# Optimization experiments

Measured on AMD Instinct MI355X. Metric: run time of the kernel, lower is better.

The kernel has to match this reference:

```python
import math
import jax, jax.numpy as jnp
import numpy as np

S, M, B, D, H = 256, 256, 8, 512, 8
HD = D // H
K = S + M  # key_len


def setup_inputs() -> dict:
    key = jax.random.key(0)
    ks = jax.random.split(key, 10)
    x = jax.random.normal(ks[0], (S, B, D), jnp.float32)
    memory = jax.random.normal(ks[1], (M, B, D), jnp.float32)
    rel_pos = jax.random.normal(ks[2], (K, D), jnp.float32)
    # causal mask: True means masked (key position after query position)
    q_pos = jnp.arange(S)[:, None] + M  # (S,1)
    k_pos = jnp.arange(K)[None, :]     # (1,K)
    attn_mask = jnp.broadcast_to(k_pos > q_pos, (B, S, K))
    scale = 1.0 / math.sqrt(D)
    Wq = jax.random.normal(ks[3], (D, D), jnp.float32) * scale
    Wk = jax.random.normal(ks[4], (D, D), jnp.float32) * scale
    Wv = jax.random.normal(ks[5], (D, D), jnp.float32) * scale
    Wr = jax.random.normal(ks[6], (D, D), jnp.float32) * scale
    Wo = jax.random.normal(ks[7], (D, D), jnp.float32) * scale
    u_bias = jax.random.normal(ks[8], (H, HD), jnp.float32) * 0.02
    v_bias = jax.random.normal(ks[9], (H, HD), jnp.float32) * 0.02
    return {"x": x, "memory": memory, "rel_pos": rel_pos, "attn_mask": attn_mask,
            "Wq": Wq, "Wk": Wk, "Wv": Wv, "Wr": Wr, "Wo": Wo,
            "u_bias": u_bias, "v_bias": v_bias}


def reference(x, memory, rel_pos, attn_mask, Wq, Wk, Wv, Wr, Wo, u_bias, v_bias):
    mem = jax.lax.stop_gradient(memory)
    kv = jnp.concatenate([mem, x], axis=0)  # (K, B, D)
    # projections (torch Linear: y = x @ W.T)
    q = (x @ Wq.T).reshape(S, B, H, HD).transpose(1, 2, 0, 3)   # (B,H,S,HD)
    k = (kv @ Wk.T).reshape(K, B, H, HD).transpose(1, 2, 0, 3)  # (B,H,K,HD)
    v = (kv @ Wv.T).reshape(K, B, H, HD).transpose(1, 2, 0, 3)  # (B,H,K,HD)
    r = (rel_pos[:K] @ Wr.T).reshape(K, H, HD)                  # (K,H,HD)
    # relative index gather
    q_pos = jnp.arange(S)[:, None] + M
    k_pos = jnp.arange(K)[None, :]
    rel_idx = jnp.clip(q_pos - k_pos, 0, K - 1)  # (S,K)
    r_qk = r[rel_idx]                            # (S,K,H,HD)
    qk = jnp.einsum('bhqd,bhkd->bhqk', q, k)
    qr = jnp.einsum('bhqd,qkhd->bhqk', q, r_qk)
    uk = jnp.einsum('hd,bhkd->bhk', u_bias, k)[:, :, None, :]
    vr = jnp.einsum('hd,qkhd->hqk', v_bias, r_qk)[None]
    scores = (qk + qr + uk + vr) / math.sqrt(HD)  # (B,H,S,K)
    scores = jnp.where(attn_mask[:, None, :, :], -jnp.inf, scores)
    weights = jax.nn.softmax(scores, axis=-1)
    y = jnp.einsum('bhqk,bhkd->bhqd', weights, v)
    y = y.transpose(2, 0, 1, 3).reshape(S, B, D)
    return y @ Wo.T
```

## Files before the change

kernel.cpp:

```cpp
#include <hip/hip_runtime.h>
#include <hip/hip_bf16.h>
#include <math.h>

constexpr int S_  = 256;
constexpr int Mm  = 256;
constexpr int Bb  = 8;
constexpr int Dd  = 512;
constexpr int Hh  = 8;
constexpr int HDd = 64;
constexpr int Kk  = 512;

typedef unsigned short u16;
typedef short bf16x8 __attribute__((ext_vector_type(8)));
typedef float f32x4  __attribute__((ext_vector_type(4)));

constexpr int LROW = 72;
constexpr int QSTR = 520;

__device__ __forceinline__ u16 f2b(float f) {
  __hip_bfloat16 h = __float2bfloat16(f);
  u16 b; __builtin_memcpy(&b, &h, 2); return b;
}
__device__ __forceinline__ unsigned int cvt2(float x, float y) {
  __hip_bfloat162 h = __float22bfloat162_rn(make_float2(x, y));
  unsigned int bits; __builtin_memcpy(&bits, &h, 4); return bits;
}
__device__ __forceinline__ float b2f(u16 b) {
  union { unsigned int u; float f; } v; v.u = ((unsigned int)b) << 16;
  return v.f;
}
__device__ __forceinline__ int4 pack8(float4 a, float4 b) {
  int4 r;
  r.x = (int)cvt2(a.x, a.y);
  r.y = (int)cvt2(a.z, a.w);
  r.z = (int)cvt2(b.x, b.y);
  r.w = (int)cvt2(b.z, b.w);
  return r;
}

__device__ __forceinline__ void stage_bf16(u16* dst, const u16* __restrict__ src,
                                           int ld, int tid) {
  const int r = tid >> 3, c = (tid & 7) * 8;
  *(int4*)(dst + r * LROW + c)        = *(const int4*)(src + (size_t)r * ld + c);
  *(int4*)(dst + (r + 32) * LROW + c) = *(const int4*)(src + (size_t)(r + 32) * ld + c);
}
__device__ __forceinline__ void stage_f32(u16* dst, const float* __restrict__ src,
                                          int ld, int tid, int nrow32) {
  const int r = tid >> 3, c = (tid & 7) * 8;
  for (int hh = 0; hh < nrow32; ++hh) {
    const float4 a = *(const float4*)(src + (size_t)(r + 32 * hh) * ld + c);
    const float4 b = *(const float4*)(src + (size_t)(r + 32 * hh) * ld + c + 4);
    *(int4*)(dst + (r + 32 * hh) * LROW + c) = pack8(a, b);
  }
}

__device__ __forceinline__ void mfma_step(const u16* As, const u16* Bs,
                                          f32x4 (&acc)[4], int wave, int lane) {
  const int r16 = lane & 15, q8 = (lane >> 4) * 8;
#pragma unroll
  for (int ks = 0; ks < 64; ks += 32) {
    const bf16x8 a = *(const bf16x8*)(As + (wave * 16 + r16) * LROW + ks + q8);
#pragma unroll
    for (int nb = 0; nb < 4; ++nb) {
      const bf16x8 b = *(const bf16x8*)(Bs + (nb * 16 + r16) * LROW + ks + q8);
      acc[nb] = __builtin_amdgcn_mfma_f32_16x16x32_bf16(a, b, acc[nb], 0, 0, 0);
    }
  }
}

__global__ __launch_bounds__(256) void k_proj(const float* __restrict__ x,
                                              const float* __restrict__ mem,
                                              const float* __restrict__ rel,
                                              const float* __restrict__ Wq,
                                              const float* __restrict__ Wk,
                                              const float* __restrict__ Wv,
                                              const float* __restrict__ Wr,
                                              const float* __restrict__ ub,
                                              const float* __restrict__ vb,
                                              u16* __restrict__ qu,
                                              u16* __restrict__ qv,
                                              u16* __restrict__ kb,
                                              u16* __restrict__ vT,
                                              u16* __restrict__ rT) {
  __shared__ u16 As[128 * LROW], Bs[64 * LROW], Bs2[64 * LROW];
  const int tid = threadIdx.x, wave = tid >> 6, lane = tid & 63;
  const int r16 = lane & 15, q8 = (lane >> 4) * 8, rq = (lane >> 4) * 4;
  const int sr = tid >> 3, scg = (tid & 7) * 8;
  const int bid = blockIdx.x;
  int kind, mt, nt;
  if (bid < 128)      { kind = 0; const int t = bid;       mt = t >> 3; nt = t & 7; }
  else if (bid < 384) { kind = 1; const int t = bid - 128; mt = t >> 3; nt = t & 7; }
  else                { kind = 2; const int t = bid - 384; mt = t >> 3; nt = t & 7; }
  const int m0 = mt * 128, n0 = nt * 64;
  const float *A, *B, *B2 = nullptr;
  if (kind == 0)      { A = x + (size_t)m0 * Dd; B = Wq + (size_t)n0 * Dd; }
  else if (kind == 1) { A = (m0 < Mm * Bb) ? mem + (size_t)m0 * Dd
                                           : x + (size_t)(m0 - Mm * Bb) * Dd;
                        B = Wk + (size_t)n0 * Dd; B2 = Wv + (size_t)n0 * Dd; }
  else                { A = rel + (size_t)m0 * Dd; B = Wr + (size_t)n0 * Dd; }

  f32x4 accK[2][4], accV[2][4];
#pragma unroll
  for (int mi = 0; mi < 2; ++mi)
#pragma unroll
    for (int nb = 0; nb < 4; ++nb) {
      accK[mi][nb] = (f32x4){0.f, 0.f, 0.f, 0.f};
      accV[mi][nb] = (f32x4){0.f, 0.f, 0.f, 0.f};
    }

  float4 fa[8], fb[4], fv[4];
#pragma unroll
  for (int hh = 0; hh < 4; ++hh) {
    fa[2 * hh]     = *(const float4*)(A + (size_t)(sr + 32 * hh) * Dd + scg);
    fa[2 * hh + 1] = *(const float4*)(A + (size_t)(sr + 32 * hh) * Dd + scg + 4);
  }
#pragma unroll
  for (int hh = 0; hh < 2; ++hh) {
    fb[2 * hh]     = *(const float4*)(B + (size_t)(sr + 32 * hh) * Dd + scg);
    fb[2 * hh + 1] = *(const float4*)(B + (size_t)(sr + 32 * hh) * Dd + scg + 4);
  }
  if (kind == 1) {
#pragma unroll
    for (int hh = 0; hh < 2; ++hh) {
      fv[2 * hh]     = *(const float4*)(B2 + (size_t)(sr + 32 * hh) * Dd + scg);
      fv[2 * hh + 1] = *(const float4*)(B2 + (size_t)(sr + 32 * hh) * Dd + scg + 4);
    }
  }
#pragma unroll
  for (int hh = 0; hh < 4; ++hh)
    *(int4*)(As + (sr + 32 * hh) * LROW + scg) = pack8(fa[2 * hh], fa[2 * hh + 1]);
#pragma unroll
  for (int hh = 0; hh < 2; ++hh)
    *(int4*)(Bs + (sr + 32 * hh) * LROW + scg) = pack8(fb[2 * hh], fb[2 * hh + 1]);
  if (kind == 1) {
#pragma unroll
    for (int hh = 0; hh < 2; ++hh)
      *(int4*)(Bs2 + (sr + 32 * hh) * LROW + scg) = pack8(fv[2 * hh], fv[2 * hh + 1]);
  }
  __syncthreads();

  for (int k0 = 0; k0 < Dd; k0 += 64) {
    const bool more = k0 < Dd - 64;
    if (more) {
      const int kn = k0 + 64;
#pragma unroll
      for (int hh = 0; hh < 4; ++hh) {
        fa[2 * hh]     = *(const float4*)(A + (size_t)(sr + 32 * hh) * Dd + kn + scg);
        fa[2 * hh + 1] = *(const float4*)(A + (size_t)(sr + 32 * hh) * Dd + kn + scg + 4);
      }
#pragma unroll
      for (int hh = 0; hh < 2; ++hh) {
        fb[2 * hh]     = *(const float4*)(B + (size_t)(sr + 32 * hh) * Dd + kn + scg);
        fb[2 * hh + 1] = *(const float4*)(B + (size_t)(sr + 32 * hh) * Dd + kn + scg + 4);
      }
      if (kind == 1) {
#pragma unroll
        for (int hh = 0; hh < 2; ++hh) {
          fv[2 * hh]     = *(const float4*)(B2 + (size_t)(sr + 32 * hh) * Dd + kn + scg);
          fv[2 * hh + 1] = *(const float4*)(B2 + (size_t)(sr + 32 * hh) * Dd + kn + scg + 4);
        }
      }
    }
#pragma unroll
    for (int ks = 0; ks < 64; ks += 32) {
      bf16x8 a[2];
#pragma unroll
      for (int mi = 0; mi < 2; ++mi)
        a[mi] = *(const bf16x8*)(As + (wave * 32 + mi * 16 + r16) * LROW + ks + q8);
#pragma unroll
      for (int nb = 0; nb < 4; ++nb) {
        const bf16x8 bk = *(const bf16x8*)(Bs + (nb * 16 + r16) * LROW + ks + q8);
#pragma unroll
        for (int mi = 0; mi < 2; ++mi)
          accK[mi][nb] = __builtin_amdgcn_mfma_f32_16x16x32_bf16(a[mi], bk, accK[mi][nb], 0, 0, 0);
        if (kind == 1) {
          const bf16x8 bv = *(const bf16x8*)(Bs2 + (nb * 16 + r16) * LROW + ks + q8);
#pragma unroll
          for (int mi = 0; mi < 2; ++mi)
            accV[mi][nb] = __builtin_amdgcn_mfma_f32_16x16x32_bf16(a[mi], bv, accV[mi][nb], 0, 0, 0);
        }
      }
    }
    __syncthreads();
    if (more) {
#pragma unroll
      for (int hh = 0; hh < 4; ++hh)
        *(int4*)(As + (sr + 32 * hh) * LROW + scg) = pack8(fa[2 * hh], fa[2 * hh + 1]);
#pragma unroll
      for (int hh = 0; hh < 2; ++hh)
        *(int4*)(Bs + (sr + 32 * hh) * LROW + scg) = pack8(fb[2 * hh], fb[2 * hh + 1]);
      if (kind == 1) {
#pragma unroll
        for (int hh = 0; hh < 2; ++hh)
          *(int4*)(Bs2 + (sr + 32 * hh) * LROW + scg) = pack8(fv[2 * hh], fv[2 * hh + 1]);
      }
      __syncthreads();
    }
  }

  const int h = n0 >> 6;
  if (kind == 0) {
#pragma unroll
    for (int nb = 0; nb < 4; ++nb) {
      const int hd = nb * 16 + r16, n = n0 + hd;
      const float u = ub[n], v = vb[n];
#pragma unroll
      for (int mi = 0; mi < 2; ++mi)
#pragma unroll
        for (int r = 0; r < 4; ++r) {
          const int m = m0 + wave * 32 + mi * 16 + rq + r;
          const int s = m >> 3, b = m & 7;
          const size_t d = ((size_t)(b * Hh + h) * S_ + s) * HDd + hd;
          qu[d] = f2b(accK[mi][nb][r] + u);
          qv[d] = f2b(accK[mi][nb][r] + v);
        }
    }
  } else if (kind == 1) {
#pragma unroll
    for (int nb = 0; nb < 4; ++nb) {
      const int hd = nb * 16 + r16;
#pragma unroll
      for (int mi = 0; mi < 2; ++mi)
#pragma unroll
        for (int r = 0; r < 4; ++r) {
          const int m = m0 + wave * 32 + mi * 16 + rq + r;
          const int pos = m >> 3, b = m & 7;
          kb[((size_t)(b * Hh + h) * Kk + pos) * HDd + hd] = f2b(accK[mi][nb][r]);
          vT[((size_t)(b * Hh + h) * HDd + hd) * Kk + pos] = f2b(accV[mi][nb][r]);
        }
    }
  } else {
#pragma unroll
    for (int nb = 0; nb < 4; ++nb) {
      const int hd = nb * 16 + r16;
#pragma unroll
      for (int mi = 0; mi < 2; ++mi)
#pragma unroll
        for (int r = 0; r < 4; ++r) {
          const int j = m0 + wave * 32 + mi * 16 + rq + r;
          rT[((size_t)h * Kk + j) * HDd + hd] = f2b(accK[mi][nb][r]);
        }
    }
  }
}

__global__ __launch_bounds__(256) void k_attn(const u16* __restrict__ qu,
                                              const u16* __restrict__ qv,
                                              const u16* __restrict__ kb,
                                              const u16* __restrict__ vT,
                                              const u16* __restrict__ rT,
                                              u16* __restrict__ y) {
  extern __shared__ u16 lds[];
  u16* QRP = lds;
  u16* bufs0 = lds + 64 * QSTR;
  u16* bufs1 = bufs0 + 64 * LROW;
  u16* bufs2 = bufs1 + 64 * LROW;
  u16* bufs[3] = {bufs0, bufs1, bufs2};
  const int tid = threadIdx.x, wave = tid >> 6, lane = tid & 63;
  const int q0 = blockIdx.x * 64, bh = blockIdx.y, h = bh & 7, b = bh >> 3;
  const int r16 = lane & 15, q8 = (lane >> 4) * 8, rq = (lane >> 4) * 4;
  const int sr = tid >> 3, scg = (tid & 7) * 8;

  const u16* qvp = qv + ((size_t)bh * S_ + q0 + wave * 16 + r16) * HDd;
  const bf16x8 av0 = *(const bf16x8*)(qvp + q8);
  const bf16x8 av1 = *(const bf16x8*)(qvp + 32 + q8);
  const u16* qup = qu + ((size_t)bh * S_ + q0 + wave * 16 + r16) * HDd;
  const bf16x8 au0 = *(const bf16x8*)(qup + q8);
  const bf16x8 au1 = *(const bf16x8*)(qup + 32 + q8);

  const u16* rbase = rT + (size_t)h * Kk * HDd;
  const u16* kbase = kb + (size_t)bh * Kk * HDd;
  const u16* vbase = vT + (size_t)bh * HDd * Kk;

  auto tsrc = [&](int jj, const u16*& s, int& ld) {
    if (jj < 8)       { s = rbase + (size_t)(jj * 64) * HDd;       ld = HDd; }
    else if (jj < 16) { s = kbase + (size_t)((jj - 8) * 64) * HDd; ld = HDd; }
    else              { s = vbase + (jj - 16) * 64;                ld = Kk;  }
  };

  f32x4 sc[8][4];
  f32x4 o[4];
#pragma unroll
  for (int nb = 0; nb < 4; ++nb) o[nb] = (f32x4){0.f, 0.f, 0.f, 0.f};
  float mx[4]  = {-INFINITY, -INFINITY, -INFINITY, -INFINITY};

  *(int4*)(bufs0 + sr * LROW + scg) =
      *(const int4*)(rbase + (size_t)sr * HDd + scg);
  *(int4*)(bufs0 + (sr + 32) * LROW + scg) =
      *(const int4*)(rbase + (size_t)(sr + 32) * HDd + scg);
  int4 Rc0, Rc1;
  {
    const u16* s; int ld; tsrc(1, s, ld);
    Rc0 = *(const int4*)(s + (size_t)sr * ld + scg);
    Rc1 = *(const int4*)(s + (size_t)(sr + 32) * ld + scg);
  }
  __syncthreads();

#pragma unroll
  for (int j = 0; j < 24; ++j) {
    int4 Rn0, Rn1;
    if (j < 22) {
      const u16* s; int ld; tsrc(j + 2, s, ld);
      Rn0 = *(const int4*)(s + (size_t)sr * ld + scg);
      Rn1 = *(const int4*)(s + (size_t)(sr + 32) * ld + scg);
    }
    if (j < 23) {
      u16* d = bufs[(j + 1) % 3];
      *(int4*)(d + sr * LROW + scg)        = Rc0;
      *(int4*)(d + (sr + 32) * LROW + scg) = Rc1;
    }
    const u16* buf = bufs[j % 3];

    if (j < 8) {
      f32x4 c4[4];
#pragma unroll
      for (int nb = 0; nb < 4; ++nb) c4[nb] = (f32x4){0.f, 0.f, 0.f, 0.f};
#pragma unroll
      for (int ks = 0; ks < 64; ks += 32) {
        const bf16x8 a = ks ? av1 : av0;
#pragma unroll
        for (int nb = 0; nb < 4; ++nb) {
          const bf16x8 bb = *(const bf16x8*)(buf + (nb * 16 + r16) * LROW + ks + q8);
          c4[nb] = __builtin_amdgcn_mfma_f32_16x16x32_bf16(a, bb, c4[nb], 0, 0, 0);
        }
      }
#pragma unroll
      for (int nb = 0; nb < 4; ++nb)
#pragma unroll
        for (int r = 0; r < 4; ++r)
          QRP[(wave * 16 + rq + r) * QSTR + j * 64 + nb * 16 + r16] = f2b(c4[nb][r]);
    } else if (j < 16) {
      const int t = j - 8;
#pragma unroll
      for (int nb = 0; nb < 4; ++nb) sc[t][nb] = (f32x4){0.f, 0.f, 0.f, 0.f};
#pragma unroll
      for (int ks = 0; ks < 64; ks += 32) {
        const bf16x8 a = ks ? au1 : au0;
#pragma unroll
        for (int nb = 0; nb < 4; ++nb) {
          const bf16x8 bb = *(const bf16x8*)(buf + (nb * 16 + r16) * LROW + ks + q8);
          sc[t][nb] = __builtin_amdgcn_mfma_f32_16x16x32_bf16(a, bb, sc[t][nb], 0, 0, 0);
        }
      }
      if (j == 15) {
#pragma unroll
        for (int kt = 0; kt < 8; ++kt)
#pragma unroll
          for (int nb = 0; nb < 4; ++nb) {
            const int kk = kt * 64 + nb * 16 + r16;
#pragma unroll
            for (int r = 0; r < 4; ++r) {
              const int ql = wave * 16 + rq + r;
              const int q  = q0 + ql;
              float v;
              if (kk <= q + Mm) {
                const float qr = b2f(QRP[ql * QSTR + (q + Mm - kk)]);
                v = (sc[kt][nb][r] + qr) * 0.125f;
              } else {
                v = -INFINITY;
              }
              sc[kt][nb][r] = v;
              mx[r] = fmaxf(mx[r], v);
            }
          }
#pragma unroll
        for (int r = 0; r < 4; ++r)
#pragma unroll
          for (int off = 1; off < 16; off <<= 1)
            mx[r] = fmaxf(mx[r], __shfl_xor(mx[r], off));
        float sum[4] = {0.f, 0.f, 0.f, 0.f};
#pragma unroll
        for (int kt = 0; kt < 8; ++kt)
#pragma unroll
          for (int nb = 0; nb < 4; ++nb)
#pragma unroll
            for (int r = 0; r < 4; ++r) {
              const float p = __expf(sc[kt][nb][r] - mx[r]);
              sc[kt][nb][r] = p;
              sum[r] += p;
            }
#pragma unroll
        for (int r = 0; r < 4; ++r)
#pragma unroll
          for (int off = 1; off < 16; off <<= 1) sum[r] += __shfl_xor(sum[r], off);
        float inv[4];
#pragma unroll
        for (int r = 0; r < 4; ++r) inv[r] = 1.0f / sum[r];
#pragma unroll
        for (int kt = 0; kt < 8; ++kt)
#pragma unroll
          for (int nb = 0; nb < 4; ++nb)
#pragma unroll
            for (int r = 0; r < 4; ++r)
              QRP[(wave * 16 + rq + r) * QSTR + kt * 64 + nb * 16 + r16] =
                  f2b(sc[kt][nb][r] * inv[r]);
      }
    } else {
      const int t = j - 16;
#pragma unroll
      for (int ks = 0; ks < 64; ks += 32) {
        const bf16x8 a = *(const bf16x8*)(QRP + (wave * 16 + r16) * QSTR + t * 64 + ks + q8);
#pragma unroll
        for (int nb = 0; nb < 4; ++nb) {
          const bf16x8 bb = *(const bf16x8*)(buf + (nb * 16 + r16) * LROW + ks + q8);
          o[nb] = __builtin_amdgcn_mfma_f32_16x16x32_bf16(a, bb, o[nb], 0, 0, 0);
        }
      }
    }

    __syncthreads();
    Rc0 = Rn0; Rc1 = Rn1;
  }

#pragma unroll
  for (int nb = 0; nb < 4; ++nb) {
    const int hd = nb * 16 + r16;
#pragma unroll
    for (int r = 0; r < 4; ++r) {
      const int q = q0 + wave * 16 + rq + r;
      y[((size_t)q * Bb + b) * Dd + h * HDd + hd] = f2b(o[nb][r]);
    }
  }
}

__global__ __launch_bounds__(256) void k_out(const u16* __restrict__ y,
                                             const float* __restrict__ Wo,
                                             float* __restrict__ out) {
  __shared__ u16 As[2][64 * LROW], Bs[2][64 * LROW];
  const int tid = threadIdx.x, wave = tid >> 6, lane = tid & 63;
  const int n0 = blockIdx.x * 64, m0 = blockIdx.y * 64;
  const int sr = tid >> 3, scg = (tid & 7) * 8;
  const u16* Ay = y + (size_t)m0 * Dd;
  const float* Bw = Wo + (size_t)n0 * Dd;
  f32x4 acc[4];
#pragma unroll
  for (int i = 0; i < 4; ++i) acc[i] = (f32x4){0.f, 0.f, 0.f, 0.f};

  stage_bf16(As[0], Ay, Dd, tid);
  stage_f32(Bs[0], Bw, Dd, tid, 2);
  __syncthreads();

#pragma unroll
  for (int t = 0; t < 8; ++t) {
    int4 La0, La1;
    float4 f0, f1, f2, f3;
    if (t < 7) {
      const u16* s = Ay + (t + 1) * 64;
      La0 = *(const int4*)(s + (size_t)sr * Dd + scg);
      La1 = *(const int4*)(s + (size_t)(sr + 32) * Dd + scg);
      const float* w = Bw + (t + 1) * 64;
      f0 = *(const float4*)(w + (size_t)sr * Dd + scg);
      f1 = *(const float4*)(w + (size_t)sr * Dd + scg + 4);
      f2 = *(const float4*)(w + (size_t)(sr + 32) * Dd + scg);
      f3 = *(const float4*)(w + (size_t)(sr + 32) * Dd + scg + 4);
    }
    mfma_step(As[t & 1], Bs[t & 1], acc, wave, lane);
    if (t < 7) {
      u16* da = As[(t + 1) & 1];
      *(int4*)(da + sr * LROW + scg)        = La0;
      *(int4*)(da + (sr + 32) * LROW + scg) = La1;
      u16* db = Bs[(t + 1) & 1];
      *(int4*)(db + sr * LROW + scg)        = pack8(f0, f1);
      *(int4*)(db + (sr + 32) * LROW + scg) = pack8(f2, f3);
    }
    __syncthreads();
  }

  const int r16 = lane & 15, rq = (lane >> 4) * 4;
#pragma unroll
  for (int nb = 0; nb < 4; ++nb) {
    const int n = n0 + nb * 16 + r16;
#pragma unroll
    for (int r = 0; r < 4; ++r) {
      const int m = m0 + wave * 16 + rq + r;
      out[(size_t)m * Dd + n] = acc[nb][r];
    }
  }
}

extern "C" void kernel_launch(void* const* d_in, const int* in_sizes, int n_in,
                              void* d_out, int out_size, void* d_ws, size_t ws_size,
                              hipStream_t stream) {
  const float* x    = (const float*)d_in[0];
  const float* mem  = (const float*)d_in[1];
  const float* rel  = (const float*)d_in[2];
  const float* Wq = (const float*)d_in[4];
  const float* Wk = (const float*)d_in[5];
  const float* Wv = (const float*)d_in[6];
  const float* Wr = (const float*)d_in[7];
  const float* Wo = (const float*)d_in[8];
  const float* ub = (const float*)d_in[9];
  const float* vb = (const float*)d_in[10];
  float* out = (float*)d_out;

  u16* qu = (u16*)d_ws;
  u16* qv = qu + 1048576;
  u16* kb = qv + 1048576;
  u16* vT = kb + 2097152;
  u16* rT = vT + 2097152;
  u16* yb = rT + 262144;

  constexpr int ATTN_LDS = (64 * QSTR + 3 * 64 * LROW) * (int)sizeof(u16);
  (void)hipFuncSetAttribute((const void*)k_attn,
                            hipFuncAttributeMaxDynamicSharedMemorySize, ATTN_LDS);

  k_proj<<<dim3(416),   dim3(256), 0,        stream>>>(x, mem, rel, Wq, Wk, Wv, Wr,
                                                       ub, vb, qu, qv, kb, vT, rT);
  k_attn<<<dim3(4, 64), dim3(256), ATTN_LDS, stream>>>(qu, qv, kb, vT, rT, yb);
  k_out <<<dim3(8, 32), dim3(256), 0,        stream>>>(yb, Wo, out);
}
```

Before: 134.6 us.

## Give each wave private double-buffered LDS tiles and drop block barriers

The three-buffer LDS ring shared by the whole block is replaced with a private double buffer per wave. Each wave now loads the full 64x64 R/K/V tile itself, at eight 16-byte loads per lane, so the per-iteration __syncthreads calls can be removed. The aim is to stop the four waves from stalling on each other across the 24 pipeline steps. In exchange, global/L2 load traffic and LDS writes rise fourfold, register pressure goes up, and the kernel's LDS footprint grows substantially.

```diff
diff --git a/kernel.cpp b/kernel.cpp
--- a/kernel.cpp
+++ b/kernel.cpp
@@ -252,14 +252,12 @@
                                               u16* __restrict__ y) {
   extern __shared__ u16 lds[];
   u16* QRP = lds;
-  u16* bufs0 = lds + 64 * QSTR;
-  u16* bufs1 = bufs0 + 64 * LROW;
-  u16* bufs2 = bufs1 + 64 * LROW;
-  u16* bufs[3] = {bufs0, bufs1, bufs2};
   const int tid = threadIdx.x, wave = tid >> 6, lane = tid & 63;
+  u16* wb0 = lds + 64 * QSTR + wave * (2 * 64 * LROW);
+  u16* wb1 = wb0 + 64 * LROW;
   const int q0 = blockIdx.x * 64, bh = blockIdx.y, h = bh & 7, b = bh >> 3;
   const int r16 = lane & 15, q8 = (lane >> 4) * 8, rq = (lane >> 4) * 4;
-  const int sr = tid >> 3, scg = (tid & 7) * 8;
+  const int sr8 = lane >> 3, sc8 = (lane & 7) * 8;
 
   const u16* qvp = qv + ((size_t)bh * S_ + q0 + wave * 16 + r16) * HDd;
   const bf16x8 av0 = *(const bf16x8*)(qvp + q8);
@@ -284,32 +282,37 @@
   for (int nb = 0; nb < 4; ++nb) o[nb] = (f32x4){0.f, 0.f, 0.f, 0.f};
   float mx[4]  = {-INFINITY, -INFINITY, -INFINITY, -INFINITY};
 
-  *(int4*)(bufs0 + sr * LROW + scg) =
-      *(const int4*)(rbase + (size_t)sr * HDd + scg);
-  *(int4*)(bufs0 + (sr + 32) * LROW + scg) =
-      *(const int4*)(rbase + (size_t)(sr + 32) * HDd + scg);
-  int4 Rc0, Rc1;
+  {
+    const u16* s; int ld; tsrc(0, s, ld);
+#pragma unroll
+    for (int g = 0; g < 8; ++g) {
+      const int rr = sr8 + 8 * g;
+      *(int4*)(wb0 + rr * LROW + sc8) = *(const int4*)(s + (size_t)rr * ld + sc8);
+    }
+  }
+  int4 R[8];
   {
     const u16* s; int ld; tsrc(1, s, ld);
-    Rc0 = *(const int4*)(s + (size_t)sr * ld + scg);
-    Rc1 = *(const int4*)(s + (size_t)(sr + 32) * ld + scg);
-  }
-  __syncthreads();
+#pragma unroll
+    for (int g = 0; g < 8; ++g)
+      R[g] = *(const int4*)(s + (size_t)(sr8 + 8 * g) * ld + sc8);
+  }
 
 #pragma unroll
   for (int j = 0; j < 24; ++j) {
-    int4 Rn0, Rn1;
+    const u16* buf = (j & 1) ? wb1 : wb0;
+    u16* nxt = (j & 1) ? wb0 : wb1;
+    if (j < 23) {
+#pragma unroll
+      for (int g = 0; g < 8; ++g)
+        *(int4*)(nxt + (sr8 + 8 * g) * LROW + sc8) = R[g];
+    }
     if (j < 22) {
       const u16* s; int ld; tsrc(j + 2, s, ld);
-      Rn0 = *(const int4*)(s + (size_t)sr * ld + scg);
-      Rn1 = *(const int4*)(s + (size_t)(sr + 32) * ld + scg);
-    }
-    if (j < 23) {
-      u16* d = bufs[(j + 1) % 3];
-      *(int4*)(d + sr * LROW + scg)        = Rc0;
-      *(int4*)(d + (sr + 32) * LROW + scg) = Rc1;
-    }
-    const u16* buf = bufs[j % 3];
+#pragma unroll
+      for (int g = 0; g < 8; ++g)
+        R[g] = *(const int4*)(s + (size_t)(sr8 + 8 * g) * ld + sc8);
+    }
 
     if (j < 8) {
       f32x4 c4[4];
@@ -407,9 +410,6 @@
         }
       }
     }
-
-    __syncthreads();
-    Rc0 = Rn0; Rc1 = Rn1;
   }
 
 #pragma unroll
@@ -500,7 +500,7 @@
   u16* rT = vT + 2097152;
   u16* yb = rT + 262144;
 
-  constexpr int ATTN_LDS = (64 * QSTR + 3 * 64 * LROW) * (int)sizeof(u16);
+  constexpr int ATTN_LDS = (64 * QSTR + 4 * 2 * 64 * LROW) * (int)sizeof(u16);
   (void)hipFuncSetAttribute((const void*)k_attn,
                             hipFuncAttributeMaxDynamicSharedMemorySize, ATTN_LDS);
 
```

New measurement: 176.6 us. 1.31x slower.
